# Kernel tuning notes

Measured on AMD Instinct MI355X. Metric: run time of the kernel, lower is better.

## Reference

```python
import jax, jax.numpy as jnp
import numpy as np


def _hfft3(x):
    # sequential Hermitian FFT along the 3 spatial axes; each axis n -> 2*(n-1)
    for ax in (2, 3, 4):
        x = jnp.fft.hfft(x, axis=ax)
    return x


def _ihfft3(x):
    # sequential inverse Hermitian FFT; ihfft requires real input, so take real
    # part before each application (mirrors numpy semantics on the original code)
    for ax in (2, 3, 4):
        x = jnp.fft.ihfft(jnp.real(x), axis=ax)
    return x


def setup_inputs() -> dict:
    key = jax.random.key(0)
    k1, k2 = jax.random.split(key)
    B, Cin, Cout = 4, 32, 32
    D1 = D2 = D3 = 64
    m1 = m2 = m3 = 16
    scale = 1.0 / (Cin * Cout)
    x = jax.random.normal(k1, (B, Cin, D1, D2, D3), dtype=jnp.float32)
    weights1 = scale * jax.random.uniform(k2, (Cin, Cout, m1, m2, m3), dtype=jnp.float32)
    return {"x": x, "weights1": weights1}


def reference(x, weights1):
    B = x.shape[0]
    D1, D2, D3 = x.shape[2], x.shape[3], x.shape[4]
    Cout = weights1.shape[1]
    m1, m2, m3 = weights1.shape[2], weights1.shape[3], weights1.shape[4]

    # 3D Hartley-style transform: [B,Cin,2(D1-1),2(D2-1),2(D3-1)] real
    x_ht = _hfft3(x)

    # mode truncation + channel mixing on low modes only
    low = jnp.einsum("bixyz,ioxyz->boxyz", x_ht[:, :, :m1, :m2, :m3], weights1)

    out_ht = jnp.zeros((B, Cout, D1, D2, D3 // 2 + 1), dtype=x.dtype)
    out_ht = out_ht.at[:, :, :m1, :m2, :m3].set(low)

    # inverse transform -> complex [B,Cout,D1//2+1,D2//2+1,(D3//2+1)//2+1]
    out = _ihfft3(out_ht)
    # return real/imag stacked so output is real-valued
    return jnp.stack([out.real, out.imag], axis=-1)
```

## Files before the change

kernel.cpp:

```cpp
#include <hip/hip_runtime.h>


#define PI2 6.283185307179586476925f

__global__ void k_init(float* __restrict__ Tmat, float* __restrict__ cA,
                       float* __restrict__ cB, float* __restrict__ sB) {
    int t = blockIdx.x * 256 + threadIdx.x;
    if (t < 1024) {
        int k = t >> 6, j = t & 63;
        float w = (j == 0 || j == 63) ? 1.f : 2.f;
        int r = (j * k) % 126;
        Tmat[t] = w * cosf(PI2 * (float)r / 126.f);
    }
    if (t < 528) {
        int p = t >> 4, j = t & 15;
        int r = (j * p) % 64;
        cA[t] = cosf(PI2 * (float)r / 64.f) * (1.f / 64.f);
    }
    if (t < 272) {
        int p = t >> 4, j = t & 15;
        int r = (j * p) % 33;
        float a = PI2 * (float)r / 33.f;
        cB[t] = cosf(a) * (1.f / 33.f);
        sB[t] = sinf(a) * (1.f / 33.f);
    }
}

__global__ __launch_bounds__(256) void k_fwd12(const float* __restrict__ x,
                                               const float* __restrict__ Tmat,
                                               float* __restrict__ A2) {
    __shared__ float xt[64 * 68];
    __shared__ float Ts[16 * 68];
    __shared__ float tmp[16 * 68];
    const int j1 = blockIdx.x, bc = blockIdx.y;
    const int t = threadIdx.x;

    float4* xt4 = (float4*)xt;
    float4* Ts4 = (float4*)Ts;
    const float4* xg = (const float4*)(x + ((size_t)bc * 64 + j1) * 4096);
    for (int c = t; c < 1024; c += 256) {
        int j2 = c >> 4, q = c & 15;
        xt4[j2 * 17 + q] = xg[c];
    }
    if (t < 256) {
        const float4* Tg = (const float4*)Tmat;
        int k = t >> 4, q = t & 15;
        Ts4[k * 17 + q] = Tg[t];
    }
    __syncthreads();

    {
        const int j2 = (t & 15) + 16 * (t >> 6);
        const int k3b = (t >> 4) & 3;
        float acc[4] = {0.f, 0.f, 0.f, 0.f};
#pragma unroll 4
        for (int q = 0; q < 16; q++) {
            float4 xv = xt4[j2 * 17 + q];
#pragma unroll
            for (int c = 0; c < 4; c++) {
                float4 tv = Ts4[(k3b + 4 * c) * 17 + q];
                acc[c] += xv.x * tv.x + xv.y * tv.y + xv.z * tv.z + xv.w * tv.w;
            }
        }
#pragma unroll
        for (int c = 0; c < 4; c++)
            tmp[(k3b + 4 * c) * 68 + j2] = acc[c];
    }
    __syncthreads();

    {
        const int k3 = t & 15;
        const int k2 = t >> 4;
        const float4* tmp4 = (const float4*)tmp;
        float acc = 0.f;
#pragma unroll 4
        for (int q = 0; q < 16; q++) {
            float4 tv = tmp4[k3 * 17 + q];
            float4 Tv = Ts4[k2 * 17 + q];
            acc += tv.x * Tv.x + tv.y * Tv.y + tv.z * Tv.z + tv.w * Tv.w;
        }
        A2[((size_t)bc * 64 + j1) * 256 + t] = acc;
    }
}

__global__ __launch_bounds__(256) void k_fwd3(const float* __restrict__ A2,
                                              const float* __restrict__ Tmat,
                                              float* __restrict__ X) {
    __shared__ float Tst[512];
    const int k1h = blockIdx.x;
    const int bc = blockIdx.y;
    const int t = threadIdx.x;
    for (int c0 = t; c0 < 512; c0 += 256) {
        int j1 = c0 >> 3, c = c0 & 7;
        Tst[c0] = Tmat[(size_t)(k1h * 8 + c) * 64 + j1];
    }
    __syncthreads();
    const float* Ap = A2 + (size_t)bc * 64 * 256 + t;
    float acc[8] = {0.f, 0.f, 0.f, 0.f, 0.f, 0.f, 0.f, 0.f};
#pragma unroll 8
    for (int j1 = 0; j1 < 64; j1++) {
        float v = Ap[j1 * 256];
        float4 t0 = *(const float4*)&Tst[j1 * 8];
        float4 t1 = *(const float4*)&Tst[j1 * 8 + 4];
        acc[0] += v * t0.x; acc[1] += v * t0.y; acc[2] += v * t0.z; acc[3] += v * t0.w;
        acc[4] += v * t1.x; acc[5] += v * t1.y; acc[6] += v * t1.z; acc[7] += v * t1.w;
    }
    float* Xp = X + (size_t)bc * 4096 + (size_t)(k1h * 8) * 256 + t;
#pragma unroll
    for (int c = 0; c < 8; c++) Xp[(size_t)c * 256] = acc[c];
}

__global__ __launch_bounds__(256) void k_mix(const float* __restrict__ X,
                                             const float* __restrict__ W,
                                             float* __restrict__ low) {
    const int mc = blockIdx.x;
    const int o = blockIdx.y;
    const int m = mc * 256 + threadIdx.x;
    const float* Xp = X + m;
    const float* Wp = W + (size_t)o * 4096 + m;
    float acc[4] = {0.f, 0.f, 0.f, 0.f};
#pragma unroll 4
    for (int i = 0; i < 32; i++) {
        float wv = Wp[(size_t)i * 32 * 4096];
#pragma unroll
        for (int b = 0; b < 4; b++)
            acc[b] += Xp[(size_t)(b * 32 + i) * 4096] * wv;
    }
#pragma unroll
    for (int b = 0; b < 4; b++)
        low[((size_t)(b * 32 + o)) * 4096 + m] = acc[b];
}

__global__ __launch_bounds__(256) void k_inv(const float* __restrict__ low,
                                             const float* __restrict__ cA,
                                             const float* __restrict__ cB,
                                             const float* __restrict__ sB,
                                             float* __restrict__ out) {
    __shared__ float lt[4096];
    __shared__ float c1[256];
    __shared__ float c2[528];
    __shared__ float cAs[528], cBs[272], sBs[272];
    const int p1 = blockIdx.x, bo = blockIdx.y;
    const int t = threadIdx.x;

    float4* lt4 = (float4*)lt;
    const float4* lg = (const float4*)(low + (size_t)bo * 4096);
    for (int c = t; c < 1024; c += 256) lt4[c] = lg[c];
    for (int c = t; c < 528; c += 256) cAs[c] = cA[c];
    for (int c = t; c < 272; c += 256) { cBs[c] = cB[c]; sBs[c] = sB[c]; }
    __syncthreads();

    {
        float acc = 0.f;
#pragma unroll
        for (int k1 = 0; k1 < 16; k1++) acc += lt[(k1 << 8) + t] * cAs[p1 * 16 + k1];
        c1[t] = acc;
    }
    __syncthreads();

    for (int idx = t; idx < 528; idx += 256) {
        int p2 = idx >> 4, k3 = idx & 15;
        float acc = 0.f;
#pragma unroll
        for (int k2 = 0; k2 < 16; k2++) acc += c1[(k2 << 4) + k3] * cAs[p2 * 16 + k2];
        c2[idx] = acc;
    }
    __syncthreads();

    float* op = out + ((size_t)bo * 33 + p1) * 33 * 17 * 2;
    for (int idx = t; idx < 1122; idx += 256) {
        int p2 = idx / 34, rem = idx % 34;
        int p3 = rem >> 1, cc = rem & 1;
        const float* M = cc ? sBs : cBs;
        float acc = 0.f;
#pragma unroll
        for (int k3 = 0; k3 < 16; k3++) acc += c2[(p2 << 4) + k3] * M[p3 * 16 + k3];
        op[idx] = acc;
    }
}

extern "C" void kernel_launch(void* const* d_in, const int* in_sizes, int n_in,
                              void* d_out, int out_size, void* d_ws, size_t ws_size,
                              hipStream_t stream) {
    const float* x = (const float*)d_in[0];
    const float* W = (const float*)d_in[1];
    float* out = (float*)d_out;

    float* ws = (float*)d_ws;
    float* Tmat = ws;
    float* cA   = ws + 1024;
    float* cB   = ws + 1552;
    float* sB   = ws + 1824;
    float* A2   = ws + 4096;
    float* X    = A2 + 2097152;
    float* low  = X + 524288;

    k_init<<<dim3(4), dim3(256), 0, stream>>>(Tmat, cA, cB, sB);
    k_fwd12<<<dim3(64, 128), dim3(256), 0, stream>>>(x, Tmat, A2);
    k_fwd3<<<dim3(2, 128), dim3(256), 0, stream>>>(A2, Tmat, X);
    k_mix<<<dim3(16, 32), dim3(256), 0, stream>>>(X, W, low);
    k_inv<<<dim3(33, 128), dim3(256), 0, stream>>>(low, cA, cB, sB, out);
}
```

Before: 243.3 us.

## Fold init kernel into transforms and register-block fwd, mix and inverse stages

Removes the separate init kernel. Each k_fwd12 and k_fwd3 block now computes its twiddle table in-kernel, and block (0,0) of k_fwd12 writes the inverse cos/sin tables that k_inv reads later. The first k_fwd12 contraction uses a 2x2 register tile, k_mix computes two output channels per thread to reuse X loads, and k_inv handles three p1 slices per block to reuse the loaded low-mode tile. The trade is one fewer launch and less redundant global traffic against recomputing cosf per block and running fewer, heavier blocks.

```diff
diff --git a/kernel.cpp b/kernel.cpp
--- a/kernel.cpp
+++ b/kernel.cpp
@@ -3,32 +3,11 @@
 
 #define PI2 6.283185307179586476925f
 
-__global__ void k_init(float* __restrict__ Tmat, float* __restrict__ cA,
-                       float* __restrict__ cB, float* __restrict__ sB) {
-    int t = blockIdx.x * 256 + threadIdx.x;
-    if (t < 1024) {
-        int k = t >> 6, j = t & 63;
-        float w = (j == 0 || j == 63) ? 1.f : 2.f;
-        int r = (j * k) % 126;
-        Tmat[t] = w * cosf(PI2 * (float)r / 126.f);
-    }
-    if (t < 528) {
-        int p = t >> 4, j = t & 15;
-        int r = (j * p) % 64;
-        cA[t] = cosf(PI2 * (float)r / 64.f) * (1.f / 64.f);
-    }
-    if (t < 272) {
-        int p = t >> 4, j = t & 15;
-        int r = (j * p) % 33;
-        float a = PI2 * (float)r / 33.f;
-        cB[t] = cosf(a) * (1.f / 33.f);
-        sB[t] = sinf(a) * (1.f / 33.f);
-    }
-}
-
 __global__ __launch_bounds__(256) void k_fwd12(const float* __restrict__ x,
-                                               const float* __restrict__ Tmat,
-                                               float* __restrict__ A2) {
+                                               float* __restrict__ A2,
+                                               float* __restrict__ cA,
+                                               float* __restrict__ cB,
+                                               float* __restrict__ sB) {
     __shared__ float xt[64 * 68];
     __shared__ float Ts[16 * 68];
     __shared__ float tmp[16 * 68];
@@ -42,29 +21,54 @@
         int j2 = c >> 4, q = c & 15;
         xt4[j2 * 17 + q] = xg[c];
     }
-    if (t < 256) {
-        const float4* Tg = (const float4*)Tmat;
+    {
         int k = t >> 4, q = t & 15;
-        Ts4[k * 17 + q] = Tg[t];
-    }
-    __syncthreads();
-
-    {
-        const int j2 = (t & 15) + 16 * (t >> 6);
-        const int k3b = (t >> 4) & 3;
-        float acc[4] = {0.f, 0.f, 0.f, 0.f};
+        float4 tv;
+        float* tp = (float*)&tv;
+#pragma unroll
+        for (int e = 0; e < 4; e++) {
+            int j = 4 * q + e;
+            float w = (j == 0 || j == 63) ? 1.f : 2.f;
+            int r = (j * k) % 126;
+            tp[e] = w * cosf(PI2 * (float)r / 126.f);
+        }
+        Ts4[k * 17 + q] = tv;
+    }
+    if (j1 == 0 && bc == 0) {
+        for (int c = t; c < 528; c += 256) {
+            int p = c >> 4, j = c & 15;
+            int r = (j * p) % 64;
+            cA[c] = cosf(PI2 * (float)r / 64.f) * (1.f / 64.f);
+        }
+        for (int c = t; c < 272; c += 256) {
+            int p = c >> 4, j = c & 15;
+            int r = (j * p) % 33;
+            float a = PI2 * (float)r / 33.f;
+            cB[c] = cosf(a) * (1.f / 33.f);
+            sB[c] = sinf(a) * (1.f / 33.f);
+        }
+    }
+    __syncthreads();
+
+    {
+        const int j2l = t & 31;
+        const int k3l = t >> 5;
+        float a00 = 0.f, a01 = 0.f, a10 = 0.f, a11 = 0.f;
 #pragma unroll 4
         for (int q = 0; q < 16; q++) {
-            float4 xv = xt4[j2 * 17 + q];
-#pragma unroll
-            for (int c = 0; c < 4; c++) {
-                float4 tv = Ts4[(k3b + 4 * c) * 17 + q];
-                acc[c] += xv.x * tv.x + xv.y * tv.y + xv.z * tv.z + xv.w * tv.w;
-            }
-        }
-#pragma unroll
-        for (int c = 0; c < 4; c++)
-            tmp[(k3b + 4 * c) * 68 + j2] = acc[c];
+            float4 x0 = xt4[j2l * 17 + q];
+            float4 x1 = xt4[(j2l + 32) * 17 + q];
+            float4 t0 = Ts4[k3l * 17 + q];
+            float4 t1 = Ts4[(k3l + 8) * 17 + q];
+            a00 += x0.x * t0.x + x0.y * t0.y + x0.z * t0.z + x0.w * t0.w;
+            a01 += x0.x * t1.x + x0.y * t1.y + x0.z * t1.z + x0.w * t1.w;
+            a10 += x1.x * t0.x + x1.y * t0.y + x1.z * t0.z + x1.w * t0.w;
+            a11 += x1.x * t1.x + x1.y * t1.y + x1.z * t1.z + x1.w * t1.w;
+        }
+        tmp[k3l * 68 + j2l] = a00;
+        tmp[(k3l + 8) * 68 + j2l] = a01;
+        tmp[k3l * 68 + j2l + 32] = a10;
+        tmp[(k3l + 8) * 68 + j2l + 32] = a11;
     }
     __syncthreads();
 
@@ -84,7 +88,6 @@
 }
 
 __global__ __launch_bounds__(256) void k_fwd3(const float* __restrict__ A2,
-                                              const float* __restrict__ Tmat,
                                               float* __restrict__ X) {
     __shared__ float Tst[512];
     const int k1h = blockIdx.x;
@@ -92,7 +95,10 @@
     const int t = threadIdx.x;
     for (int c0 = t; c0 < 512; c0 += 256) {
         int j1 = c0 >> 3, c = c0 & 7;
-        Tst[c0] = Tmat[(size_t)(k1h * 8 + c) * 64 + j1];
+        int k1 = k1h * 8 + c;
+        float w = (j1 == 0 || j1 == 63) ? 1.f : 2.f;
+        int r = (j1 * k1) % 126;
+        Tst[c0] = w * cosf(PI2 * (float)r / 126.f);
     }
     __syncthreads();
     const float* Ap = A2 + (size_t)bc * 64 * 256 + t;
@@ -114,21 +120,27 @@
                                              const float* __restrict__ W,
                                              float* __restrict__ low) {
     const int mc = blockIdx.x;
-    const int o = blockIdx.y;
+    const int og = blockIdx.y;
     const int m = mc * 256 + threadIdx.x;
     const float* Xp = X + m;
-    const float* Wp = W + (size_t)o * 4096 + m;
-    float acc[4] = {0.f, 0.f, 0.f, 0.f};
+    const float* Wp = W + (size_t)(og * 2) * 4096 + m;
+    float acc[4][2] = {{0.f,0.f},{0.f,0.f},{0.f,0.f},{0.f,0.f}};
 #pragma unroll 4
     for (int i = 0; i < 32; i++) {
-        float wv = Wp[(size_t)i * 32 * 4096];
-#pragma unroll
-        for (int b = 0; b < 4; b++)
-            acc[b] += Xp[(size_t)(b * 32 + i) * 4096] * wv;
-    }
-#pragma unroll
-    for (int b = 0; b < 4; b++)
-        low[((size_t)(b * 32 + o)) * 4096 + m] = acc[b];
+        float w0 = Wp[(size_t)(i * 32) * 4096];
+        float w1 = Wp[(size_t)(i * 32 + 1) * 4096];
+#pragma unroll
+        for (int b = 0; b < 4; b++) {
+            float xv = Xp[(size_t)(b * 32 + i) * 4096];
+            acc[b][0] += xv * w0;
+            acc[b][1] += xv * w1;
+        }
+    }
+#pragma unroll
+    for (int b = 0; b < 4; b++) {
+        low[((size_t)(b * 32 + og * 2)) * 4096 + m] = acc[b][0];
+        low[((size_t)(b * 32 + og * 2 + 1)) * 4096 + m] = acc[b][1];
+    }
 }
 
 __global__ __launch_bounds__(256) void k_inv(const float* __restrict__ low,
@@ -137,10 +149,11 @@
                                              const float* __restrict__ sB,
                                              float* __restrict__ out) {
     __shared__ float lt[4096];
-    __shared__ float c1[256];
-    __shared__ float c2[528];
+    __shared__ float c1[3 * 256];
+    __shared__ float c2[3 * 528];
     __shared__ float cAs[528], cBs[272], sBs[272];
-    const int p1 = blockIdx.x, bo = blockIdx.y;
+    const int p1b = blockIdx.x * 3;
+    const int bo = blockIdx.y;
     const int t = threadIdx.x;
 
     float4* lt4 = (float4*)lt;
@@ -151,31 +164,45 @@
     __syncthreads();
 
     {
-        float acc = 0.f;
-#pragma unroll
-        for (int k1 = 0; k1 < 16; k1++) acc += lt[(k1 << 8) + t] * cAs[p1 * 16 + k1];
-        c1[t] = acc;
+        float e0 = 0.f, e1 = 0.f, e2 = 0.f;
+#pragma unroll
+        for (int k1 = 0; k1 < 16; k1++) {
+            float v = lt[(k1 << 8) + t];
+            e0 += v * cAs[(p1b + 0) * 16 + k1];
+            e1 += v * cAs[(p1b + 1) * 16 + k1];
+            e2 += v * cAs[(p1b + 2) * 16 + k1];
+        }
+        c1[t] = e0; c1[256 + t] = e1; c1[512 + t] = e2;
     }
     __syncthreads();
 
     for (int idx = t; idx < 528; idx += 256) {
         int p2 = idx >> 4, k3 = idx & 15;
-        float acc = 0.f;
-#pragma unroll
-        for (int k2 = 0; k2 < 16; k2++) acc += c1[(k2 << 4) + k3] * cAs[p2 * 16 + k2];
-        c2[idx] = acc;
-    }
-    __syncthreads();
-
-    float* op = out + ((size_t)bo * 33 + p1) * 33 * 17 * 2;
-    for (int idx = t; idx < 1122; idx += 256) {
-        int p2 = idx / 34, rem = idx % 34;
-        int p3 = rem >> 1, cc = rem & 1;
-        const float* M = cc ? sBs : cBs;
-        float acc = 0.f;
-#pragma unroll
-        for (int k3 = 0; k3 < 16; k3++) acc += c2[(p2 << 4) + k3] * M[p3 * 16 + k3];
-        op[idx] = acc;
+        float f0 = 0.f, f1 = 0.f, f2 = 0.f;
+#pragma unroll
+        for (int k2 = 0; k2 < 16; k2++) {
+            float cv = cAs[p2 * 16 + k2];
+            int a = (k2 << 4) + k3;
+            f0 += c1[a] * cv;
+            f1 += c1[256 + a] * cv;
+            f2 += c1[512 + a] * cv;
+        }
+        c2[idx] = f0; c2[528 + idx] = f1; c2[1056 + idx] = f2;
+    }
+    __syncthreads();
+
+    for (int s = 0; s < 3; s++) {
+        float* op = out + ((size_t)bo * 33 + p1b + s) * 33 * 17 * 2;
+        const float* c2p = c2 + s * 528;
+        for (int idx = t; idx < 1122; idx += 256) {
+            int p2 = idx / 34, rem = idx - p2 * 34;
+            int p3 = rem >> 1, cc = rem & 1;
+            const float* M = cc ? sBs : cBs;
+            float acc = 0.f;
+#pragma unroll
+            for (int k3 = 0; k3 < 16; k3++) acc += c2p[(p2 << 4) + k3] * M[p3 * 16 + k3];
+            op[idx] = acc;
+        }
     }
 }
 
@@ -187,17 +214,15 @@
     float* out = (float*)d_out;
 
     float* ws = (float*)d_ws;
-    float* Tmat = ws;
-    float* cA   = ws + 1024;
-    float* cB   = ws + 1552;
-    float* sB   = ws + 1824;
+    float* cA   = ws;
+    float* cB   = ws + 528;
+    float* sB   = ws + 800;
     float* A2   = ws + 4096;
     float* X    = A2 + 2097152;
     float* low  = X + 524288;
 
-    k_init<<<dim3(4), dim3(256), 0, stream>>>(Tmat, cA, cB, sB);
-    k_fwd12<<<dim3(64, 128), dim3(256), 0, stream>>>(x, Tmat, A2);
-    k_fwd3<<<dim3(2, 128), dim3(256), 0, stream>>>(A2, Tmat, X);
-    k_mix<<<dim3(16, 32), dim3(256), 0, stream>>>(X, W, low);
-    k_inv<<<dim3(33, 128), dim3(256), 0, stream>>>(low, cA, cB, sB, out);
-}
+    k_fwd12<<<dim3(64, 128), dim3(256), 0, stream>>>(x, A2, cA, cB, sB);
+    k_fwd3<<<dim3(2, 128), dim3(256), 0, stream>>>(A2, X);
+    k_mix<<<dim3(16, 16), dim3(256), 0, stream>>>(X, W, low);
+    k_inv<<<dim3(11, 128), dim3(256), 0, stream>>>(low, cA, cB, sB, out);
+}
```

Result: no change. 239.2 us (-1.7%).
